# Kernel optimization log

Measured on AMD Instinct MI355X. Metric: run time of the kernel, lower is better.

Reference implementation:

```python
import jax, jax.numpy as jnp
import numpy as np

DIM_Q, DIM_K, DIM_V, H = 256, 256, 384, 6
B, N = 8, 1024
NEG = -10.0 ** 10  # matches torch's (1 - A) * -10**10


def sparsemax(z):
    # simplex projection along last axis (Martins & Astudillo 2016)
    z = z - jnp.max(z, axis=-1, keepdims=True)  # shift-invariant, for fp stability
    z_sorted = jnp.flip(jnp.sort(z, axis=-1), axis=-1)          # descending
    k = jnp.arange(1, z.shape[-1] + 1, dtype=z.dtype)
    z_cumsum = jnp.cumsum(z_sorted, axis=-1)
    support = (1.0 + k * z_sorted) > z_cumsum
    k_z = jnp.sum(support, axis=-1, keepdims=True)              # int32 support size >= 1
    tau = (jnp.take_along_axis(z_cumsum, k_z - 1, axis=-1) - 1.0) / k_z.astype(z.dtype)
    return jnp.maximum(z - tau, 0.0)


def setup_inputs() -> dict:
    key = jax.random.key(0)
    ks = jax.random.split(key, 7)
    Q = jax.random.normal(ks[0], (B, N, DIM_Q), jnp.float32)
    V = jax.random.normal(ks[1], (B, N, DIM_K), jnp.float32)
    # binary adjacency mask with self-loops so every row has support
    A = jax.random.bernoulli(ks[2], 0.05, (B, N, N)).astype(jnp.float32)
    A = A.at[:, jnp.arange(N), jnp.arange(N)].set(1.0)
    # torch.nn.Linear default init: U(-1/sqrt(fan_in), 1/sqrt(fan_in)); weights stored pre-transposed [in, out]
    sq = 1.0 / np.sqrt(DIM_Q)
    sk = 1.0 / np.sqrt(DIM_K)
    WQ = jax.random.uniform(ks[3], (DIM_Q, DIM_V), jnp.float32, -sq, sq)
    bQ = jax.random.uniform(ks[4], (DIM_V,), jnp.float32, -sq, sq)
    WK = jax.random.uniform(ks[5], (DIM_K, DIM_V), jnp.float32, -sk, sk)
    bK = jax.random.uniform(ks[6], (DIM_V,), jnp.float32, -sk, sk)
    return {"Q": Q, "V": V, "A": A, "WQ": WQ, "bQ": bQ, "WK": WK, "bK": bK}


def reference(Q, V, A, WQ, bQ, WK, bK):
    b, n, _ = Q.shape
    d = DIM_V // H
    # project and split heads (torch split along dim=2 == reshape [b,n,H,d])
    q = (Q @ WQ + bQ).reshape(b, n, H, d).transpose(0, 2, 1, 3)   # [b,H,n,d]
    k = (V @ WK + bK).reshape(b, n, H, d).transpose(0, 2, 1, 3)   # [b,H,n,d]
    scale = 1.0 / jnp.sqrt(jnp.float32(DIM_V))
    logits = jnp.einsum('bhnd,bhmd->bhnm', q, k) * scale + (1.0 - A)[:, None] * NEG
    O = sparsemax(logits)                                          # [b,H,n,n], rows on simplex
    # torch: split(B) along dim0 then cat along dim2 -> head-major along last axis
    return O.transpose(0, 2, 1, 3).reshape(b, n, H * n)            # [b,n,H*n]
```

## Files before the change

### kernel.cpp

```cpp
#include <hip/hip_runtime.h>
#include <hip/hip_bf16.h>
#include <stdint.h>

#define DIMK 256
#define DIMV 384
#define NSEQ 1024
#define NHEAD 6
#define ZCAP 192

typedef __attribute__((ext_vector_type(8))) short short8;
typedef __attribute__((ext_vector_type(4))) float floatx4;

__device__ __forceinline__ unsigned short f2b(float f){
  unsigned int x = __float_as_uint(f);
  return (unsigned short)((x + 0x7fffu + ((x >> 16) & 1u)) >> 16);
}
__device__ __forceinline__ unsigned int pack2(float a, float b){
  return (unsigned int)f2b(a) | ((unsigned int)f2b(b) << 16);
}
__device__ __forceinline__ float blo(unsigned int u){ return __uint_as_float(u << 16); }

__global__ __launch_bounds__(256) void fused_pre_kernel(
    const float* __restrict__ Q, const float* __restrict__ V,
    const float* __restrict__ WQ, const float* __restrict__ WK,
    const float* __restrict__ bQ, const float* __restrict__ bK,
    const float* __restrict__ A,
    unsigned short* __restrict__ qhi, unsigned short* __restrict__ qlo,
    unsigned short* __restrict__ kf,
    unsigned long long* __restrict__ bm, unsigned short* __restrict__ bmp)
{
  int bid = blockIdx.x;
  if (bid >= 1024){
    int r = (bid - 1024) * 4 + (threadIdx.x >> 6);
    int lane = threadIdx.x & 63;
    const float* arow = A + (size_t)r * NSEQ;
    unsigned long long myw = 0;
    #pragma unroll
    for (int c = 0; c < 16; ++c){
      unsigned long long m = __ballot(arow[c * 64 + lane] > 0.5f);
      if (lane == c) myw = m;
    }
    int own = (lane < 16) ? __popcll(myw) : 0;
    int inc = own;
    #pragma unroll
    for (int o = 1; o < 16; o <<= 1){
      int t = __shfl_up(inc, o, 16);
      if ((lane & 15) >= o) inc += t;
    }
    if (lane < 16){
      bm [(size_t)r * 16 + lane] = myw;
      bmp[(size_t)r * 16 + lane] = (unsigned short)(inc - own);
    }
    return;
  }

  __shared__ uint4 lA[512];
  __shared__ unsigned short lB16[96 * 72];
  int which = bid >> 9;
  int rem = bid & 511;
  int bx = rem >> 2, by = rem & 3;
  const float* X = which ? V : Q;
  const float* W = which ? WK : WQ;
  const float* bias = which ? bK : bQ;

  int t = threadIdx.x;
  int lane = t & 63, wave = t >> 6;
  int wm = wave >> 1, wn = wave & 1;
  int rb = bx * 64;
  int nb = by * 96;
  floatx4 acc[2][3];
  #pragma unroll
  for (int mi = 0; mi < 2; ++mi)
    #pragma unroll
    for (int ni = 0; ni < 3; ++ni) acc[mi][ni] = (floatx4){0.f, 0.f, 0.f, 0.f};

  for (int it = 0; it < 4; ++it){
    int k0 = it * 64;
    #pragma unroll
    for (int i = 0; i < 2; ++i){
      int c = t + i * 256;
      int kc = c >> 6, row = c & 63;
      const float* src = X + (size_t)(rb + row) * DIMK + k0 + kc * 8;
      float4 f0 = *(const float4*)src;
      float4 f1 = *(const float4*)(src + 4);
      uint4 w;
      w.x = pack2(f0.x, f0.y); w.y = pack2(f0.z, f0.w);
      w.z = pack2(f1.x, f1.y); w.w = pack2(f1.z, f1.w);
      lA[c] = w;
    }
    #pragma unroll
    for (int i = 0; i < 6; ++i){
      int c = t + i * 256;
      int kk2 = c / 24, f4 = c % 24;
      float4 wv = *(const float4*)(W + (size_t)(k0 + kk2) * DIMV + nb + f4 * 4);
      int n0 = f4 * 4;
      lB16[(n0    ) * 72 + kk2] = f2b(wv.x);
      lB16[(n0 + 1) * 72 + kk2] = f2b(wv.y);
      lB16[(n0 + 2) * 72 + kk2] = f2b(wv.z);
      lB16[(n0 + 3) * 72 + kk2] = f2b(wv.w);
    }
    __syncthreads();
    #pragma unroll
    for (int kk = 0; kk < 2; ++kk){
      int kc  = kk * 4 + (lane >> 4);
      int r16 = lane & 15;
      short8 af[2], bf[3];
      #pragma unroll
      for (int mi = 0; mi < 2; ++mi)
        af[mi] = *(const short8*)&lA[kc * 64 + wm * 32 + mi * 16 + r16];
      #pragma unroll
      for (int ni = 0; ni < 3; ++ni)
        bf[ni] = *(const short8*)&lB16[(wn * 48 + ni * 16 + r16) * 72 + kc * 8];
      #pragma unroll
      for (int mi = 0; mi < 2; ++mi)
        #pragma unroll
        for (int ni = 0; ni < 3; ++ni)
          acc[mi][ni] = __builtin_amdgcn_mfma_f32_16x16x32_bf16(af[mi], bf[ni], acc[mi][ni], 0, 0, 0);
    }
    __syncthreads();
  }
  const float scale = 0.05103103630798288f;
  int r16 = lane & 15, rq = lane >> 4;
  #pragma unroll
  for (int ni = 0; ni < 3; ++ni){
    int col = nb + wn * 48 + ni * 16 + r16;
    float bv = bias[col];
    int h = col >> 6, d = col & 63;
    #pragma unroll
    for (int mi = 0; mi < 2; ++mi){
      #pragma unroll
      for (int q = 0; q < 4; ++q){
        int row = rb + wm * 32 + mi * 16 + rq * 4 + q;
        int bb = row >> 10, n = row & 1023;
        int slice = bb * NHEAD + h;
        size_t dst = ((((size_t)slice * 2 + (d >> 5)) * 64 + (n >> 4)) * 64
                      + ((d >> 3) & 3) * 16 + (n & 15)) * 8 + (d & 7);
        float v = acc[mi][ni][q] + bv;
        if (which){
          kf[dst] = f2b(v);
        } else {
          v *= scale;
          unsigned short hi_ = f2b(v);
          qhi[dst] = hi_;
          qlo[dst] = f2b(v - blo((unsigned int)hi_));
        }
      }
    }
  }
}

__device__ __forceinline__ void red2(float& a, float& b){
  #pragma unroll
  for (int o = 1; o < 64; o <<= 1){ a += __shfl_xor(a, o); b += __shfl_xor(b, o); }
}
__device__ __forceinline__ void red4(float& a, float& b, float& c, float& d){
  #pragma unroll
  for (int o = 1; o < 64; o <<= 1){
    a += __shfl_xor(a, o); b += __shfl_xor(b, o);
    c += __shfl_xor(c, o); d += __shfl_xor(d, o);
  }
}

__global__ __launch_bounds__(512) void attn_kernel(
    const unsigned short* __restrict__ qhi, const unsigned short* __restrict__ qlo,
    const unsigned short* __restrict__ kf, const unsigned long long* __restrict__ bm,
    const unsigned short* __restrict__ bmp, float* __restrict__ out)
{
  __shared__ unsigned long long mw[16][16];
  __shared__ unsigned short    mp[16][16];
  __shared__ float             zlds[16][ZCAP + 1];

  int bid = blockIdx.x;
  int x = bid & 7;
  int u = bid >> 3;
  int h = u >> 6;
  int rb = u & 63;
  int tid = threadIdx.x;
  int lane = tid & 63, w = tid >> 6;
  int slice = x * NHEAD + h;
  int rowbase = (x << 10) + (rb << 4);

  if (tid < 256){
    int rr = tid >> 4, ww = tid & 15;
    mw[rr][ww] = bm [((size_t)(rowbase + rr)) * 16 + ww];
    mp[rr][ww] = bmp[((size_t)(rowbase + rr)) * 16 + ww];
  }

  const short8* qh8 = (const short8*)qhi;
  const short8* ql8 = (const short8*)qlo;
  const short8* kf8 = (const short8*)kf;
  size_t ab0 = (((size_t)slice * 2 + 0) * 64 + rb) * 64 + lane;
  size_t ab1 = (((size_t)slice * 2 + 1) * 64 + rb) * 64 + lane;
  short8 ah0 = qh8[ab0], al0 = ql8[ab0];
  short8 ah1 = qh8[ab1], al1 = ql8[ab1];
  __syncthreads();

  __builtin_amdgcn_s_setprio(1);
  #pragma unroll
  for (int i = 0; i < 8; ++i){
    int tt = (w << 3) + i;
    short8 b0 = kf8[(((size_t)slice * 2 + 0) * 64 + tt) * 64 + lane];
    short8 b1 = kf8[(((size_t)slice * 2 + 1) * 64 + tt) * 64 + lane];
    floatx4 a = (floatx4){0.f, 0.f, 0.f, 0.f};
    a = __builtin_amdgcn_mfma_f32_16x16x32_bf16(al0, b0, a, 0, 0, 0);
    a = __builtin_amdgcn_mfma_f32_16x16x32_bf16(ah0, b0, a, 0, 0, 0);
    a = __builtin_amdgcn_mfma_f32_16x16x32_bf16(al1, b1, a, 0, 0, 0);
    a = __builtin_amdgcn_mfma_f32_16x16x32_bf16(ah1, b1, a, 0, 0, 0);
    int colb = (w << 7) + (i << 4) + (lane & 15);
    int cw = colb >> 6, cb = colb & 63;
    unsigned long long below = (1ull << cb) - 1ull;
    #pragma unroll
    for (int reg = 0; reg < 4; ++reg){
      int rowz = ((lane >> 4) << 2) + reg;
      unsigned long long word = mw[rowz][cw];
      if ((word >> cb) & 1){
        int rank = (int)mp[rowz][cw] + __popcll(word & below);
        if (rank < ZCAP) zlds[rowz][rank] = a[reg];
      }
    }
  }
  __builtin_amdgcn_s_setprio(0);
  __syncthreads();

  int row0 = w * 2, row1 = w * 2 + 1;
  int M0 = (int)mp[row0][15] + __popcll(mw[row0][15]);
  int M1 = (int)mp[row1][15] + __popcll(mw[row1][15]);
  float tau0, tau1;

  if (M0 <= 64 && M1 <= 64){
    bool a0 = lane < M0, a1 = lane < M1;
    float z0 = a0 ? zlds[row0][lane] : 0.f;
    float z1 = a1 ? zlds[row1][lane] : 0.f;
    float s0 = z0, s1 = z1;
    red2(s0, s1);
    tau0 = (s0 - 1.f) / (float)M0;
    tau1 = (s1 - 1.f) / (float)M1;
    int p0 = M0, p1 = M1;
    #pragma unroll 1
    for (int it = 0; it < 32; ++it){
      bool i0 = a0 && z0 > tau0, i1 = a1 && z1 > tau1;
      int n0 = __popcll(__ballot(i0));
      int n1 = __popcll(__ballot(i1));
      s0 = i0 ? z0 : 0.f; s1 = i1 ? z1 : 0.f;
      red2(s0, s1);
      bool stable = (n0 == p0) && (n1 == p1);
      tau0 = (s0 - 1.f) / (float)n0;
      tau1 = (s1 - 1.f) / (float)n1;
      p0 = n0; p1 = n1;
      if (stable) break;
    }
  } else {
    float z0a = (lane < M0)       ? zlds[row0][lane]       : 0.f;
    float z1a = (lane < M1)       ? zlds[row1][lane]       : 0.f;
    float z0b = (64 + lane < M0)  ? zlds[row0][64 + lane]  : 0.f;
    float z1b = (64 + lane < M1)  ? zlds[row1][64 + lane]  : 0.f;
    float z0c = (128 + lane < M0) ? zlds[row0][128 + lane] : 0.f;
    float z1c = (128 + lane < M1) ? zlds[row1][128 + lane] : 0.f;
    bool a0 = lane < M0, b0_ = 64 + lane < M0, c0_ = 128 + lane < M0;
    bool a1 = lane < M1, b1_ = 64 + lane < M1, c1_ = 128 + lane < M1;
    float s0 = (a0 ? z0a : 0.f) + (b0_ ? z0b : 0.f) + (c0_ ? z0c : 0.f);
    float n0 = (a0 ? 1.f : 0.f) + (b0_ ? 1.f : 0.f) + (c0_ ? 1.f : 0.f);
    float s1 = (a1 ? z1a : 0.f) + (b1_ ? z1b : 0.f) + (c1_ ? z1c : 0.f);
    float n1 = (a1 ? 1.f : 0.f) + (b1_ ? 1.f : 0.f) + (c1_ ? 1.f : 0.f);
    red4(s0, n0, s1, n1);
    tau0 = (s0 - 1.f) / n0; tau1 = (s1 - 1.f) / n1;
    float p0 = n0, p1 = n1;
    #pragma unroll 1
    for (int it = 0; it < 32; ++it){
      bool i0a = a0 && z0a > tau0, i0b = b0_ && z0b > tau0, i0c = c0_ && z0c > tau0;
      bool i1a = a1 && z1a > tau1, i1b = b1_ && z1b > tau1, i1c = c1_ && z1c > tau1;
      s0 = (i0a ? z0a : 0.f) + (i0b ? z0b : 0.f) + (i0c ? z0c : 0.f);
      n0 = (i0a ? 1.f : 0.f) + (i0b ? 1.f : 0.f) + (i0c ? 1.f : 0.f);
      s1 = (i1a ? z1a : 0.f) + (i1b ? z1b : 0.f) + (i1c ? z1c : 0.f);
      n1 = (i1a ? 1.f : 0.f) + (i1b ? 1.f : 0.f) + (i1c ? 1.f : 0.f);
      red4(s0, n0, s1, n1);
      bool stable = (n0 == p0) && (n1 == p1);
      tau0 = (s0 - 1.f) / n0; tau1 = (s1 - 1.f) / n1;
      p0 = n0; p1 = n1;
      if (stable) break;
    }
  }

  float* o0 = out + ((size_t)(rowbase + row0) * NHEAD + h) * NSEQ;
  float* o1 = out + ((size_t)(rowbase + row1) * NHEAD + h) * NSEQ;
  int b0v = (lane & 15) << 2;
  unsigned long long pmask = (1ull << b0v) - 1ull;
  #pragma unroll
  for (int qtr = 0; qtr < 4; ++qtr){
    int cw = (qtr << 2) + (lane >> 4);
    unsigned long long w0 = mw[row0][cw], w1 = mw[row1][cw];
    int rk0 = (int)mp[row0][cw] + __popcll(w0 & pmask);
    int rk1 = (int)mp[row1][cw] + __popcll(w1 & pmask);
    float v0[4], v1[4];
    #pragma unroll
    for (int j = 0; j < 4; ++j){
      int bit0 = (int)((w0 >> (b0v + j)) & 1ull);
      int bit1 = (int)((w1 >> (b0v + j)) & 1ull);
      v0[j] = bit0 ? fmaxf(zlds[row0][rk0] - tau0, 0.f) : 0.f;
      v1[j] = bit1 ? fmaxf(zlds[row1][rk1] - tau1, 0.f) : 0.f;
      rk0 += bit0; rk1 += bit1;
    }
    ((float4*)o0)[(qtr << 6) + lane] = make_float4(v0[0], v0[1], v0[2], v0[3]);
    ((float4*)o1)[(qtr << 6) + lane] = make_float4(v1[0], v1[1], v1[2], v1[3]);
  }
}

extern "C" void kernel_launch(void* const* d_in, const int* in_sizes, int n_in,
                              void* d_out, int out_size, void* d_ws, size_t ws_size,
                              hipStream_t stream) {
  const float* Q  = (const float*)d_in[0];
  const float* V  = (const float*)d_in[1];
  const float* A  = (const float*)d_in[2];
  const float* WQ = (const float*)d_in[3];
  const float* bQ = (const float*)d_in[4];
  const float* WK = (const float*)d_in[5];
  const float* bK = (const float*)d_in[6];
  float* out = (float*)d_out;

  char* ws = (char*)d_ws;
  unsigned short*     qhi = (unsigned short*)ws;
  unsigned short*     qlo = (unsigned short*)(ws + (size_t)6291456);
  unsigned short*     kf  = (unsigned short*)(ws + (size_t)12582912);
  unsigned long long* bm  = (unsigned long long*)(ws + (size_t)19267584);
  unsigned short*     bmp = (unsigned short*)(ws + (size_t)20316160);
  (void)in_sizes; (void)n_in; (void)out_size; (void)ws_size;

  fused_pre_kernel<<<3072, 256, 0, stream>>>(Q, V, WQ, WK, bQ, bK, A,
                                             qhi, qlo, kf, bm, bmp);
  attn_kernel<<<3072, 512, 0, stream>>>(qhi, qlo, kf, bm, bmp, out);
}
```

Before: 85.56 us.

## Split fused attention into MFMA logits kernel and separate sparsemax kernel

Splits the fused attention+sparsemax kernel in two. The first kernel computes the masked logits with MFMA and writes the compacted support values to a workspace buffer in fp16. The second kernel loads them, solves for sparsemax tau by fixed-point iteration, and writes the dense output. This targets better occupancy or scheduling in each phase, at the cost of an extra launch and a round trip through global memory. Storing logits in fp16 also loses some precision, and the split path only runs when the workspace is large enough.

```diff
diff --git a/kernel.cpp b/kernel.cpp
--- a/kernel.cpp
+++ b/kernel.cpp
@@ -1,5 +1,6 @@
 #include <hip/hip_runtime.h>
 #include <hip/hip_bf16.h>
+#include <hip/hip_fp16.h>
 #include <stdint.h>
 
 #define DIMK 256
@@ -161,14 +162,13 @@
   }
 }
 
-__global__ __launch_bounds__(512) void attn_kernel(
+__global__ __launch_bounds__(512) void attn_mfma_kernel(
     const unsigned short* __restrict__ qhi, const unsigned short* __restrict__ qlo,
     const unsigned short* __restrict__ kf, const unsigned long long* __restrict__ bm,
-    const unsigned short* __restrict__ bmp, float* __restrict__ out)
+    const unsigned short* __restrict__ bmp, __half* __restrict__ zg)
 {
   __shared__ unsigned long long mw[16][16];
   __shared__ unsigned short    mp[16][16];
-  __shared__ float             zlds[16][ZCAP + 1];
 
   int bid = blockIdx.x;
   int x = bid & 7;
@@ -186,6 +186,177 @@
     mp[rr][ww] = bmp[((size_t)(rowbase + rr)) * 16 + ww];
   }
 
+  const short8* qh8 = (const short8*)qhi;
+  const short8* ql8 = (const short8*)qlo;
+  const short8* kf8 = (const short8*)kf;
+  size_t ab0 = (((size_t)slice * 2 + 0) * 64 + rb) * 64 + lane;
+  size_t ab1 = (((size_t)slice * 2 + 1) * 64 + rb) * 64 + lane;
+  short8 ah0 = qh8[ab0], al0 = ql8[ab0];
+  short8 ah1 = qh8[ab1], al1 = ql8[ab1];
+  __syncthreads();
+
+  size_t zslice = (size_t)slice * NSEQ;
+  __builtin_amdgcn_s_setprio(1);
+  #pragma unroll
+  for (int i = 0; i < 8; ++i){
+    int tt = (w << 3) + i;
+    short8 b0 = kf8[(((size_t)slice * 2 + 0) * 64 + tt) * 64 + lane];
+    short8 b1 = kf8[(((size_t)slice * 2 + 1) * 64 + tt) * 64 + lane];
+    floatx4 a = (floatx4){0.f, 0.f, 0.f, 0.f};
+    a = __builtin_amdgcn_mfma_f32_16x16x32_bf16(al0, b0, a, 0, 0, 0);
+    a = __builtin_amdgcn_mfma_f32_16x16x32_bf16(ah0, b0, a, 0, 0, 0);
+    a = __builtin_amdgcn_mfma_f32_16x16x32_bf16(al1, b1, a, 0, 0, 0);
+    a = __builtin_amdgcn_mfma_f32_16x16x32_bf16(ah1, b1, a, 0, 0, 0);
+    int colb = (w << 7) + (i << 4) + (lane & 15);
+    int cw = colb >> 6, cb = colb & 63;
+    unsigned long long below = (1ull << cb) - 1ull;
+    #pragma unroll
+    for (int reg = 0; reg < 4; ++reg){
+      int rowz = ((lane >> 4) << 2) + reg;
+      unsigned long long word = mw[rowz][cw];
+      if ((word >> cb) & 1){
+        int rank = (int)mp[rowz][cw] + __popcll(word & below);
+        if (rank < ZCAP)
+          zg[(zslice + (rb << 4) + rowz) * ZCAP + rank] = __float2half(a[reg]);
+      }
+    }
+  }
+  __builtin_amdgcn_s_setprio(0);
+}
+
+__global__ __launch_bounds__(256) void sparsemax_kernel(
+    const __half* __restrict__ zg, const unsigned long long* __restrict__ bm,
+    const unsigned short* __restrict__ bmp, float* __restrict__ out)
+{
+  __shared__ float             zl[8][ZCAP + 1];
+  __shared__ unsigned long long mwL[8][16];
+  __shared__ unsigned short    mpL[8][16];
+
+  int bid = blockIdx.x;
+  int x = bid & 7;
+  int u = bid >> 3;
+  int h = u >> 7;
+  int rg = u & 127;
+  int tid = threadIdx.x;
+  int lane = tid & 63, w = tid >> 6;
+  int slice = x * NHEAD + h;
+  int n0 = (rg << 3) + (w << 1);
+  int l0 = (w << 1), l1 = l0 + 1;
+
+  if (lane < 32){
+    int rr = lane >> 4, wi = lane & 15;
+    size_t rowg = (size_t)(x << 10) + n0 + rr;
+    mwL[l0 + rr][wi] = bm [rowg * 16 + wi];
+    mpL[l0 + rr][wi] = bmp[rowg * 16 + wi];
+  }
+  int M0 = (int)mpL[l0][15] + __popcll(mwL[l0][15]);
+  int M1 = (int)mpL[l1][15] + __popcll(mwL[l1][15]);
+
+  size_t zb0 = ((size_t)slice * NSEQ + n0) * ZCAP;
+  size_t zb1 = zb0 + ZCAP;
+  float z0a = 0.f, z0b = 0.f, z0c = 0.f, z1a = 0.f, z1b = 0.f, z1c = 0.f;
+  if (lane < M0){ z0a = __half2float(zg[zb0 + lane]); zl[l0][lane] = z0a; }
+  if (lane < M1){ z1a = __half2float(zg[zb1 + lane]); zl[l1][lane] = z1a; }
+  if (M0 > 64 && 64 + lane < M0){ z0b = __half2float(zg[zb0 + 64 + lane]); zl[l0][64 + lane] = z0b; }
+  if (M1 > 64 && 64 + lane < M1){ z1b = __half2float(zg[zb1 + 64 + lane]); zl[l1][64 + lane] = z1b; }
+  if (M0 > 128 && 128 + lane < M0){ z0c = __half2float(zg[zb0 + 128 + lane]); zl[l0][128 + lane] = z0c; }
+  if (M1 > 128 && 128 + lane < M1){ z1c = __half2float(zg[zb1 + 128 + lane]); zl[l1][128 + lane] = z1c; }
+
+  float tau0, tau1;
+  if (M0 <= 64 && M1 <= 64){
+    bool a0 = lane < M0, a1 = lane < M1;
+    float s0 = z0a, s1 = z1a;
+    red2(s0, s1);
+    tau0 = (s0 - 1.f) / (float)M0;
+    tau1 = (s1 - 1.f) / (float)M1;
+    int p0 = M0, p1 = M1;
+    #pragma unroll 1
+    for (int it = 0; it < 32; ++it){
+      bool i0 = a0 && z0a > tau0, i1 = a1 && z1a > tau1;
+      int n0c = __popcll(__ballot(i0));
+      int n1c = __popcll(__ballot(i1));
+      s0 = i0 ? z0a : 0.f; s1 = i1 ? z1a : 0.f;
+      red2(s0, s1);
+      bool stable = (n0c == p0) && (n1c == p1);
+      tau0 = (s0 - 1.f) / (float)n0c;
+      tau1 = (s1 - 1.f) / (float)n1c;
+      p0 = n0c; p1 = n1c;
+      if (stable) break;
+    }
+  } else {
+    bool a0 = lane < M0, b0_ = 64 + lane < M0, c0_ = 128 + lane < M0;
+    bool a1 = lane < M1, b1_ = 64 + lane < M1, c1_ = 128 + lane < M1;
+    float s0 = z0a + z0b + z0c;
+    float n0c = (a0 ? 1.f : 0.f) + (b0_ ? 1.f : 0.f) + (c0_ ? 1.f : 0.f);
+    float s1 = z1a + z1b + z1c;
+    float n1c = (a1 ? 1.f : 0.f) + (b1_ ? 1.f : 0.f) + (c1_ ? 1.f : 0.f);
+    red4(s0, n0c, s1, n1c);
+    tau0 = (s0 - 1.f) / n0c; tau1 = (s1 - 1.f) / n1c;
+    float p0 = n0c, p1 = n1c;
+    #pragma unroll 1
+    for (int it = 0; it < 32; ++it){
+      bool i0a = a0 && z0a > tau0, i0b = b0_ && z0b > tau0, i0c = c0_ && z0c > tau0;
+      bool i1a = a1 && z1a > tau1, i1b = b1_ && z1b > tau1, i1c = c1_ && z1c > tau1;
+      s0 = (i0a ? z0a : 0.f) + (i0b ? z0b : 0.f) + (i0c ? z0c : 0.f);
+      n0c = (i0a ? 1.f : 0.f) + (i0b ? 1.f : 0.f) + (i0c ? 1.f : 0.f);
+      s1 = (i1a ? z1a : 0.f) + (i1b ? z1b : 0.f) + (i1c ? z1c : 0.f);
+      n1c = (i1a ? 1.f : 0.f) + (i1b ? 1.f : 0.f) + (i1c ? 1.f : 0.f);
+      red4(s0, n0c, s1, n1c);
+      bool stable = (n0c == p0) && (n1c == p1);
+      tau0 = (s0 - 1.f) / n0c; tau1 = (s1 - 1.f) / n1c;
+      p0 = n0c; p1 = n1c;
+      if (stable) break;
+    }
+  }
+
+  float* o0 = out + ((size_t)((x << 10) + n0) * NHEAD + h) * NSEQ;
+  float* o1 = o0 + (size_t)NHEAD * NSEQ;
+  int b0v = (lane & 15) << 2;
+  unsigned long long pmask = (1ull << b0v) - 1ull;
+  #pragma unroll
+  for (int qtr = 0; qtr < 4; ++qtr){
+    int cw = (qtr << 2) + (lane >> 4);
+    unsigned long long w0 = mwL[l0][cw], w1 = mwL[l1][cw];
+    int rk0 = (int)mpL[l0][cw] + __popcll(w0 & pmask);
+    int rk1 = (int)mpL[l1][cw] + __popcll(w1 & pmask);
+    float v0[4], v1[4];
+    #pragma unroll
+    for (int j = 0; j < 4; ++j){
+      int bit0 = (int)((w0 >> (b0v + j)) & 1ull);
+      int bit1 = (int)((w1 >> (b0v + j)) & 1ull);
+      v0[j] = bit0 ? fmaxf(zl[l0][rk0] - tau0, 0.f) : 0.f;
+      v1[j] = bit1 ? fmaxf(zl[l1][rk1] - tau1, 0.f) : 0.f;
+      rk0 += bit0; rk1 += bit1;
+    }
+    ((float4*)o0)[(qtr << 6) + lane] = make_float4(v0[0], v0[1], v0[2], v0[3]);
+    ((float4*)o1)[(qtr << 6) + lane] = make_float4(v1[0], v1[1], v1[2], v1[3]);
+  }
+}
+
+__global__ __launch_bounds__(512) void attn_kernel(
+    const unsigned short* __restrict__ qhi, const unsigned short* __restrict__ qlo,
+    const unsigned short* __restrict__ kf, const unsigned long long* __restrict__ bm,
+    const unsigned short* __restrict__ bmp, float* __restrict__ out)
+{
+  __shared__ unsigned long long mw[16][16];
+  __shared__ unsigned short    mp[16][16];
+  __shared__ float             zlds[16][ZCAP + 1];
+
+  int bid = blockIdx.x;
+  int x = bid & 7;
+  int u = bid >> 3;
+  int h = u >> 6;
+  int rb = u & 63;
+  int tid = threadIdx.x;
+  int lane = tid & 63, w = tid >> 6;
+  int slice = x * NHEAD + h;
+  int rowbase = (x << 10) + (rb << 4);
+
+  if (tid < 256){
+    int rr = tid >> 4, ww = tid & 15;
+    mw[rr][ww] = bm [((size_t)(rowbase + rr)) * 16 + ww];
+    mp[rr][ww] = bmp[((size_t)(rowbase + rr)) * 16 + ww];
+  }
   const short8* qh8 = (const short8*)qhi;
   const short8* ql8 = (const short8*)qlo;
   const short8* kf8 = (const short8*)kf;
@@ -323,9 +494,16 @@
   unsigned short*     kf  = (unsigned short*)(ws + (size_t)12582912);
   unsigned long long* bm  = (unsigned long long*)(ws + (size_t)19267584);
   unsigned short*     bmp = (unsigned short*)(ws + (size_t)20316160);
-  (void)in_sizes; (void)n_in; (void)out_size; (void)ws_size;
+  __half*             zg  = (__half*)(ws + (size_t)20578304);
+  const size_t WS_NEEDED_SPLIT = 20578304 + (size_t)48 * 1024 * ZCAP * 2;
+  (void)in_sizes; (void)n_in; (void)out_size;
 
   fused_pre_kernel<<<3072, 256, 0, stream>>>(Q, V, WQ, WK, bQ, bK, A,
                                              qhi, qlo, kf, bm, bmp);
-  attn_kernel<<<3072, 512, 0, stream>>>(qhi, qlo, kf, bm, bmp, out);
-}
+  if (ws_size >= WS_NEEDED_SPLIT){
+    attn_mfma_kernel<<<3072, 512, 0, stream>>>(qhi, qlo, kf, bm, bmp, zg);
+    sparsemax_kernel<<<6144, 256, 0, stream>>>(zg, bm, bmp, out);
+  } else {
+    attn_kernel<<<3072, 512, 0, stream>>>(qhi, qlo, kf, bm, bmp, out);
+  }
+}
```

After: 101.1 us. 18.1% more time.
